# Optimization experiments

Measured on AMD Instinct MI355X. Metric: run time of the kernel, lower is better.

Reference implementation:

```python
import jax, jax.numpy as jnp
import numpy as np

N_HEADS = 8
D_EMBED = 512
D_HEAD = D_EMBED // N_HEADS


def setup_inputs() -> dict:
    key = jax.random.key(0)
    ks = jax.random.split(key, 5)
    x = jax.random.normal(ks[0], (1, 4096, D_EMBED), dtype=jnp.float32)
    # in_proj: Linear(d, 3d); out_proj: Linear(d, d). Stored as [in, out] for x @ W.
    scale_in = 1.0 / np.sqrt(D_EMBED)
    W_in = jax.random.uniform(ks[1], (D_EMBED, 3 * D_EMBED), jnp.float32, -scale_in, scale_in)
    b_in = jax.random.uniform(ks[2], (3 * D_EMBED,), jnp.float32, -scale_in, scale_in)
    W_out = jax.random.uniform(ks[3], (D_EMBED, D_EMBED), jnp.float32, -scale_in, scale_in)
    b_out = jax.random.uniform(ks[4], (D_EMBED,), jnp.float32, -scale_in, scale_in)
    return {"x": x, "W_in": W_in, "b_in": b_in, "W_out": W_out, "b_out": b_out,
            "causal_mask": 1}


def reference(x, W_in, b_in, W_out, b_out, causal_mask):
    B, S, D = x.shape
    qkv = x @ W_in + b_in                      # [B, S, 3D]
    q, k, v = jnp.split(qkv, 3, axis=-1)
    # [B, S, D] -> [B, H, S, d_head]
    def split_heads(t):
        return t.reshape(B, S, N_HEADS, D_HEAD).transpose(0, 2, 1, 3)
    q, k, v = split_heads(q), split_heads(k), split_heads(v)
    weight = jnp.einsum("bhqd,bhkd->bhqk", q, k)  # [B, H, S, S]
    if causal_mask:
        mask = jnp.triu(jnp.ones((S, S), dtype=bool), k=1)
        weight = jnp.where(mask, -jnp.inf, weight)
    weight = weight / jnp.sqrt(jnp.float32(D_HEAD)).astype(weight.dtype)
    weight = jax.nn.softmax(weight, axis=-1)
    out = jnp.einsum("bhqk,bhkd->bhqd", weight, v)  # [B, H, S, d_head]
    out = out.transpose(0, 2, 1, 3).reshape(B, S, D)
    return out @ W_out + b_out
```

## Files before the change

kernel.cpp:

```cpp
#include <hip/hip_runtime.h>
#include <math.h>

#define SEQ 4096
#define DM 512
#define NH 8
#define DH 64
#define TQK (3 * DM)
#define QSCALE 0.18033688011112042f

typedef __attribute__((ext_vector_type(8))) short bf16x8;
typedef __attribute__((ext_vector_type(4))) float floatx4;
typedef unsigned short ushort_t;

__device__ __forceinline__ floatx4 mfma16(bf16x8 a, bf16x8 b, floatx4 c) {
    return __builtin_amdgcn_mfma_f32_16x16x32_bf16(a, b, c, 0, 0, 0);
}
__device__ __forceinline__ float ex2(float x) { return __builtin_amdgcn_exp2f(x); }

__device__ __forceinline__ unsigned int pk2(float a, float b) {
    unsigned int ua = __float_as_uint(a); ua = (ua + 0x7FFFu + ((ua >> 16) & 1u)) >> 16;
    unsigned int ub = __float_as_uint(b); ub = (ub + 0x7FFFu + ((ub >> 16) & 1u)) >> 16;
    return ua | (ub << 16);
}
__device__ __forceinline__ unsigned short f2bf(float x) {
    unsigned int u = __float_as_uint(x);
    return (unsigned short)((u + 0x7FFFu + ((u >> 16) & 1u)) >> 16);
}
__device__ __forceinline__ float bflo(unsigned int u) { return __uint_as_float(u << 16); }
__device__ __forceinline__ float bfhi(unsigned int u) { return __uint_as_float(u & 0xFFFF0000u); }

__device__ __forceinline__ void gload_lds16(const void* g, void* l) {
    __builtin_amdgcn_global_load_lds(
        (const __attribute__((address_space(1))) unsigned int*)g,
        (__attribute__((address_space(3))) unsigned int*)l, 16, 0, 0);
}

#define DPPMAX(x, ctrl) \
    (x) = fmaxf((x), __int_as_float(__builtin_amdgcn_update_dpp(0, __float_as_int(x), (ctrl), 0xF, 0xF, true)))
__device__ __forceinline__ float row_max16(float x) {
    DPPMAX(x, 0xB1);
    DPPMAX(x, 0x4E);
    DPPMAX(x, 0x141);
    DPPMAX(x, 0x140);
    return x;
}

__global__ __launch_bounds__(256) void prep(const float* __restrict__ x,
                                            const float* __restrict__ W_in,
                                            const float* __restrict__ W_out,
                                            ushort_t* __restrict__ xb,
                                            ushort_t* __restrict__ wti,
                                            ushort_t* __restrict__ wto) {
    __shared__ float T[64][65];
    const int bid = blockIdx.x, tid = threadIdx.x;
    if (bid < 1024) {
        const int i = bid * 256 + tid;
        const float4* p = (const float4*)x + (size_t)i * 2;
        float4 f0 = p[0], f1 = p[1];
        ((uint4*)xb)[i] = make_uint4(pk2(f0.x, f0.y), pk2(f0.z, f0.w),
                                     pk2(f1.x, f1.y), pk2(f1.z, f1.w));
        return;
    }
    const float* W; ushort_t* WT; int N, K, n0, k0; bool qscale;
    if (bid < 1216) { int id = bid - 1024; W = W_in;  WT = wti; N = TQK; K = DM;
                      n0 = (id % 24) * 64; k0 = (id / 24) * 64; qscale = true; }
    else            { int id = bid - 1216; W = W_out; WT = wto; N = DM;  K = DM;
                      n0 = (id % 8) * 64;  k0 = (id / 8) * 64;  qscale = false; }
    {
        const int r = tid >> 2, g = tid & 3;
        const float* src = W + (size_t)(k0 + r) * N + n0 + g * 16;
#pragma unroll
        for (int i = 0; i < 4; i++) {
            float4 f = ((const float4*)src)[i];
            T[g * 16 + i * 4 + 0][r] = f.x;
            T[g * 16 + i * 4 + 1][r] = f.y;
            T[g * 16 + i * 4 + 2][r] = f.z;
            T[g * 16 + i * 4 + 3][r] = f.w;
        }
    }
    __syncthreads();
    const int nr = tid >> 2, g2 = tid & 3;
    const float sc = (qscale && (n0 + nr < DM)) ? QSCALE : 1.0f;
    unsigned int pk[8];
#pragma unroll
    for (int j = 0; j < 8; j++)
        pk[j] = pk2(T[nr][g2 * 16 + 2 * j] * sc, T[nr][g2 * 16 + 2 * j + 1] * sc);
    ushort_t* dst = WT + (size_t)(n0 + nr) * K + k0 + g2 * 16;
    ((uint4*)dst)[0] = make_uint4(pk[0], pk[1], pk[2], pk[3]);
    ((uint4*)dst)[1] = make_uint4(pk[4], pk[5], pk[6], pk[7]);
}

__global__ __launch_bounds__(256) void gemm_in(const ushort_t* __restrict__ A,
                                               const ushort_t* __restrict__ BT,
                                               const float* __restrict__ bias,
                                               ushort_t* __restrict__ Cv,
                                               ushort_t* __restrict__ vt_out) {
    __shared__ __align__(16) ushort_t As[2][128 * 64];
    __shared__ __align__(16) ushort_t Bs[2][128 * 64];
    const int tid  = threadIdx.x;
    const int lane = tid & 63;
    const int w    = tid >> 6;
    const int quad = lane >> 4;
    const int ln   = lane & 15;
    const int row0 = blockIdx.y * 128;
    const int col0 = blockIdx.x * 128;
    const int wm = w >> 1, wn = w & 1;
    const int srow = lane >> 3;
    const int js   = (lane & 7) ^ srow;
    const int K = DM, N = TQK;

    floatx4 acc[4][4];
#pragma unroll
    for (int i = 0; i < 4; i++)
#pragma unroll
        for (int j = 0; j < 4; j++) acc[i][j] = (floatx4){0.f, 0.f, 0.f, 0.f};

#pragma unroll
    for (int i = 0; i < 4; i++) {
        const int c = w * 4 + i;
        gload_lds16(A  + (size_t)(row0 + c * 8 + srow) * K + js * 8, &As[0][c * 512]);
        gload_lds16(BT + (size_t)(col0 + c * 8 + srow) * K + js * 8, &Bs[0][c * 512]);
    }

    for (int kt = 0; kt < 8; kt++) {
        const int cur = kt & 1;
        __syncthreads();
        if (kt < 7) {
            const int k0n = (kt + 1) << 6;
#pragma unroll
            for (int i = 0; i < 4; i++) {
                const int c = w * 4 + i;
                gload_lds16(A  + (size_t)(row0 + c * 8 + srow) * K + k0n + js * 8, &As[cur ^ 1][c * 512]);
                gload_lds16(BT + (size_t)(col0 + c * 8 + srow) * K + k0n + js * 8, &Bs[cur ^ 1][c * 512]);
            }
        }
#pragma unroll
        for (int s = 0; s < 2; s++) {
            bf16x8 af[4], bfr[4];
#pragma unroll
            for (int i = 0; i < 4; i++) {
                const int lm = wm * 64 + i * 16 + ln;
                af[i] = *(const bf16x8*)&As[cur][lm * 64 + ((s * 4 + quad) ^ (ln & 7)) * 8];
                const int lnn = wn * 64 + i * 16 + ln;
                bfr[i] = *(const bf16x8*)&Bs[cur][lnn * 64 + ((s * 4 + quad) ^ (ln & 7)) * 8];
            }
#pragma unroll
            for (int i = 0; i < 4; i++)
#pragma unroll
                for (int j = 0; j < 4; j++)
                    acc[i][j] = mfma16(af[i], bfr[j], acc[i][j]);
        }
    }

    if (col0 >= 2 * DM) {
#pragma unroll
        for (int j = 0; j < 4; j++) {
            const int n = col0 + wn * 64 + j * 16 + ln;
            const float bv = bias[n];
#pragma unroll
            for (int i = 0; i < 4; i++) {
                const int mb = row0 + wm * 64 + i * 16 + quad * 4;
                uint2 pkd;
                pkd.x = pk2(acc[i][j][0] + bv, acc[i][j][1] + bv);
                pkd.y = pk2(acc[i][j][2] + bv, acc[i][j][3] + bv);
                *(uint2*)&vt_out[(size_t)(n - 2 * DM) * SEQ + mb] = pkd;
            }
        }
        return;
    }

#pragma unroll
    for (int j = 0; j < 4; j++) {
        const int n = col0 + wn * 64 + j * 16 + ln;
        const float bv = bias[n] * ((n < DM) ? QSCALE : 1.0f);
#pragma unroll
        for (int i = 0; i < 4; i++) {
            const int mb = row0 + wm * 64 + i * 16 + quad * 4;
#pragma unroll
            for (int r = 0; r < 4; r++)
                Cv[(size_t)(mb + r) * N + n] = f2bf(acc[i][j][r] + bv);
        }
    }
}

__global__ __launch_bounds__(512) void attn_split(const ushort_t* __restrict__ qkv_b,
                                                  const ushort_t* __restrict__ vt,
                                                  ushort_t* __restrict__ po,
                                                  float2* __restrict__ pml) {
    __shared__ __align__(16) ushort_t Ks[2][64 * 64];
    __shared__ __align__(16) ushort_t Vs[2][64 * 64];
    __shared__ __align__(16) ushort_t Ps[128 * 72];

    const int tid  = threadIdx.x;
    const int lane = tid & 63;
    const int w    = tid >> 6;
    const int quad = lane >> 4;
    const int ln   = lane & 15;
    const int h    = blockIdx.y;

    const int e = 143 - (int)blockIdx.x;
    int g = 0;
    while (e >= 2 * (g + 1) * (g + 2)) g++;
    const int off = e - 2 * g * (g + 1);
    const int nc  = g + 1;
    const int qt  = 4 * g + off / nc;
    const int c   = off % nc;
    const int T   = 2 * qt + 2;
    const int jt0 = (c * T) / nc;
    const int jt1 = ((c + 1) * T) / nc;
    const int q0  = qt * 128;

    const ushort_t* qrow = qkv_b + (size_t)(q0 + w * 16 + ln) * TQK + h * DH;
    const bf16x8 a0 = *(const bf16x8*)(qrow + quad * 8);
    const bf16x8 a1 = *(const bf16x8*)(qrow + quad * 8 + 32);

    const short oneb = (short)0x3F80;
    const bf16x8 vone = {oneb, oneb, oneb, oneb, oneb, oneb, oneb, oneb};

    float m_q = -INFINITY;
    floatx4 o[4], ol;
#pragma unroll
    for (int t = 0; t < 4; t++) o[t] = (floatx4){0.f, 0.f, 0.f, 0.f};
    ol = (floatx4){0.f, 0.f, 0.f, 0.f};

    const int srow = lane >> 3;
    const int js   = (lane & 7) ^ srow;

    {
        const int k0 = jt0 * 64;
        gload_lds16(qkv_b + (size_t)(k0 + w * 8 + srow) * TQK + DM + h * DH + js * 8,
                    &Ks[0][w * 512]);
        gload_lds16(vt + (size_t)(h * DH + w * 8 + srow) * SEQ + k0 + js * 8,
                    &Vs[0][w * 512]);
    }

    for (int jt = jt0; jt < jt1; ++jt) {
        const int cur = (jt - jt0) & 1;
        const int k0  = jt * 64;
        __syncthreads();
        if (jt + 1 < jt1) {
            const int k0n = (jt + 1) * 64;
            gload_lds16(qkv_b + (size_t)(k0n + w * 8 + srow) * TQK + DM + h * DH + js * 8,
                        &Ks[cur ^ 1][w * 512]);
            gload_lds16(vt + (size_t)(h * DH + w * 8 + srow) * SEQ + k0n + js * 8,
                        &Vs[cur ^ 1][w * 512]);
        }

        floatx4 sa[4];
#pragma unroll
        for (int t = 0; t < 4; t++) {
            const int n = t * 16 + ln;
            const bf16x8 b0 = *(const bf16x8*)&Ks[cur][n * 64 + ((quad) ^ (ln & 7)) * 8];
            const bf16x8 b1 = *(const bf16x8*)&Ks[cur][n * 64 + ((4 + quad) ^ (ln & 7)) * 8];
            floatx4 acc = {0.f, 0.f, 0.f, 0.f};
            acc = mfma16(a0, b0, acc);
            acc = mfma16(a1, b1, acc);
            sa[t] = acc;
        }

        if (k0 + 63 > q0 + w * 16) {
#pragma unroll
            for (int t = 0; t < 4; t++) {
                const int cg2 = k0 + t * 16 + ln;
#pragma unroll
                for (int r = 0; r < 4; r++) {
                    const int rg = q0 + w * 16 + quad * 4 + r;
                    if (cg2 > rg) sa[t][r] = -INFINITY;
                }
            }
        }

        float mx = sa[0][0];
#pragma unroll
        for (int t = 0; t < 4; t++)
#pragma unroll
            for (int r = 0; r < 4; r++) mx = fmaxf(mx, sa[t][r]);
        mx = row_max16(mx);
        const float mn = fmaxf(fmaxf(m_q, mx), -1e30f);
        const float alpha = ex2(m_q - mn);
        m_q = mn;
#pragma unroll
        for (int t = 0; t < 4; t++)
#pragma unroll
            for (int r = 0; r < 4; r++) {
                const float p = ex2(sa[t][r] - mn);
                Ps[(w * 16 + quad * 4 + r) * 72 + t * 16 + ln] =
                    (ushort_t)(__float_as_uint(p) >> 16);
            }
        if (alpha < 1.0f) {
#pragma unroll
            for (int t = 0; t < 4; t++)
#pragma unroll
                for (int r = 0; r < 4; r++) o[t][r] *= alpha;
#pragma unroll
            for (int r = 0; r < 4; r++) ol[r] *= alpha;
        }

        __builtin_amdgcn_wave_barrier();

        const bf16x8 p0 = *(const bf16x8*)&Ps[(w * 16 + ln) * 72 + quad * 8];
        const bf16x8 p1 = *(const bf16x8*)&Ps[(w * 16 + ln) * 72 + quad * 8 + 32];
#pragma unroll
        for (int t = 0; t < 4; t++) {
            const int d = t * 16 + ln;
            const bf16x8 v0 = *(const bf16x8*)&Vs[cur][d * 64 + ((quad) ^ (ln & 7)) * 8];
            const bf16x8 v1 = *(const bf16x8*)&Vs[cur][d * 64 + ((4 + quad) ^ (ln & 7)) * 8];
            o[t] = mfma16(p0, v0, o[t]);
            o[t] = mfma16(p1, v1, o[t]);
        }
        ol = mfma16(p0, vone, ol);
        ol = mfma16(p1, vone, ol);
    }

    const size_t pbase  = ((size_t)h * 144 + e) * (128 * 64);
    const size_t mlbase = ((size_t)h * 144 + e) * 128;
#pragma unroll
    for (int t = 0; t < 4; t++)
#pragma unroll
        for (int r = 0; r < 4; r++)
            po[pbase + (size_t)(w * 16 + quad * 4 + r) * 64 + t * 16 + ln] = f2bf(o[t][r]);
    if (ln == 0) {
#pragma unroll
        for (int r = 0; r < 4; r++)
            pml[mlbase + w * 16 + quad * 4 + r] = make_float2(m_q, ol[r]);
    }
}

__global__ __launch_bounds__(512) void gemm_out(const ushort_t* __restrict__ po,
                                                const float2* __restrict__ pml,
                                                const ushort_t* __restrict__ BT,
                                                const float* __restrict__ bias,
                                                float* __restrict__ out) {
    __shared__ __align__(16) ushort_t As[2][128 * 72];
    __shared__ __align__(16) ushort_t Bs[2][128 * 64];
    const int tid  = threadIdx.x;
    const int lane = tid & 63;
    const int w    = tid >> 6;
    const int quad = lane >> 4;
    const int ln   = lane & 15;
    const int row0 = blockIdx.y * 128;
    const int col0 = blockIdx.x * 128;
    const int wm = w >> 2, wn = w & 3;
    const int srow = lane >> 3;
    const int js   = (lane & 7) ^ srow;

    const int qt = blockIdx.y;
    const int gq = qt >> 2;
    const int nc = gq + 1;
    const int sbase = 2 * gq * (gq + 1) + (qt & 3) * nc;

    const int cr = tid >> 2, cg = tid & 3;

    floatx4 acc[4][2];
#pragma unroll
    for (int i = 0; i < 4; i++)
#pragma unroll
        for (int j = 0; j < 2; j++) acc[i][j] = (floatx4){0.f, 0.f, 0.f, 0.f};

    auto combine = [&](int head, int buf) {
        float2 ml[8];
        float M = -INFINITY;
        for (int ci = 0; ci < nc; ci++) {
            ml[ci] = pml[((size_t)head * 144 + sbase + ci) * 128 + cr];
            M = fmaxf(M, ml[ci].x);
        }
        float L = 0.f;
        float a[16];
#pragma unroll
        for (int j = 0; j < 16; j++) a[j] = 0.f;
        for (int ci = 0; ci < nc; ci++) {
            const float wgt = ex2(ml[ci].x - M);
            L += wgt * ml[ci].y;
            const ushort_t* p = po + ((size_t)head * 144 + sbase + ci) * (128 * 64)
                                   + (size_t)cr * 64 + cg * 16;
            uint4 u0 = ((const uint4*)p)[0];
            uint4 u1 = ((const uint4*)p)[1];
            const unsigned int uu[8] = {u0.x, u0.y, u0.z, u0.w, u1.x, u1.y, u1.z, u1.w};
#pragma unroll
            for (int j = 0; j < 8; j++) {
                a[2 * j]     += wgt * bflo(uu[j]);
                a[2 * j + 1] += wgt * bfhi(uu[j]);
            }
        }
        const float inv = 1.0f / L;
        unsigned int pk[8];
#pragma unroll
        for (int j = 0; j < 8; j++)
            pk[j] = pk2(a[2 * j] * inv, a[2 * j + 1] * inv);
        uint4* dst = (uint4*)&As[buf][cr * 72 + cg * 16];
        dst[0] = make_uint4(pk[0], pk[1], pk[2], pk[3]);
        dst[1] = make_uint4(pk[4], pk[5], pk[6], pk[7]);
    };
    auto loadB = [&](int kt, int buf) {
#pragma unroll
        for (int i = 0; i < 2; i++) {
            const int cgrp = w * 2 + i;
            gload_lds16(BT + (size_t)(col0 + cgrp * 8 + srow) * DM + kt * 64 + js * 8,
                        &Bs[buf][cgrp * 512]);
        }
    };

    loadB(0, 0);
    combine(0, 0);

    for (int kt = 0; kt < 8; kt++) {
        const int cur = kt & 1;
        __syncthreads();
        if (kt < 7) {
            loadB(kt + 1, cur ^ 1);
            combine(kt + 1, cur ^ 1);
        }
#pragma unroll
        for (int s = 0; s < 2; s++) {
            bf16x8 af[4], bfr[2];
#pragma unroll
            for (int i = 0; i < 4; i++) {
                const int lm = wm * 64 + i * 16 + ln;
                af[i] = *(const bf16x8*)&As[cur][lm * 72 + (s * 4 + quad) * 8];
            }
#pragma unroll
            for (int j = 0; j < 2; j++) {
                const int lnn = wn * 32 + j * 16 + ln;
                bfr[j] = *(const bf16x8*)&Bs[cur][lnn * 64 + ((s * 4 + quad) ^ (ln & 7)) * 8];
            }
#pragma unroll
            for (int i = 0; i < 4; i++)
#pragma unroll
                for (int j = 0; j < 2; j++)
                    acc[i][j] = mfma16(af[i], bfr[j], acc[i][j]);
        }
    }

#pragma unroll
    for (int j = 0; j < 2; j++) {
        const int n = col0 + wn * 32 + j * 16 + ln;
        const float bv = bias[n];
#pragma unroll
        for (int i = 0; i < 4; i++) {
            const int mb = row0 + wm * 64 + i * 16 + quad * 4;
#pragma unroll
            for (int r = 0; r < 4; r++)
                out[(size_t)(mb + r) * DM + n] = acc[i][j][r] + bv;
        }
    }
}

extern "C" void kernel_launch(void* const* d_in, const int* in_sizes, int n_in,
                              void* d_out, int out_size, void* d_ws, size_t ws_size,
                              hipStream_t stream) {
    const float* x     = (const float*)d_in[0];
    const float* W_in  = (const float*)d_in[1];
    const float* b_in  = (const float*)d_in[2];
    const float* W_out = (const float*)d_in[3];
    const float* b_out = (const float*)d_in[4];
    float* out = (float*)d_out;

    char* ws = (char*)d_ws;
    ushort_t* xb    = (ushort_t*)ws;
    ushort_t* wti   = (ushort_t*)(ws + (4u  << 20));
    ushort_t* wto   = (ushort_t*)(ws + (6u  << 20));
    ushort_t* qkv_b = (ushort_t*)(ws + (7u  << 20));
    ushort_t* vtb   = (ushort_t*)(ws + (19u << 20));
    ushort_t* po    = (ushort_t*)(ws + (23u << 20));
    float2*   pml   = (float2*)  (ws + (42u << 20));

    prep<<<1280, 256, 0, stream>>>(x, W_in, W_out, xb, wti, wto);

    gemm_in<<<dim3(TQK / 128, SEQ / 128), 256, 0, stream>>>(xb, wti, b_in, qkv_b, vtb);

    attn_split<<<dim3(144, NH), 512, 0, stream>>>(qkv_b, vtb, po, pml);

    gemm_out<<<dim3(DM / 128, SEQ / 128), 512, 0, stream>>>(po, pml, wto, b_out, out);
}
```

Measured before the change: 173.4 us.

## Split split-KV combine out of output GEMM into separate kernel

Moves the flash-decoding style partial-result combine from inside the output projection GEMM into its own attn_combine kernel, which writes a bf16 attention output buffer. The output GEMM becomes a plain pipelined bf16 GEMM with async global-to-LDS loads for both operands, a swizzled A layout, and smaller 128x64 tiles at 256 threads, giving twice as many blocks. This is meant to stop each GEMM block from recomputing the combine serially on its critical path, and to raise parallelism. In exchange it adds a kernel launch and a round trip of the combined activations through global memory.

```diff
diff --git a/kernel.cpp b/kernel.cpp
--- a/kernel.cpp
+++ b/kernel.cpp
@@ -326,89 +326,99 @@
     }
 }
 
-__global__ __launch_bounds__(512) void gemm_out(const ushort_t* __restrict__ po,
-                                                const float2* __restrict__ pml,
+__global__ __launch_bounds__(512) void attn_combine(const ushort_t* __restrict__ po,
+                                                    const float2* __restrict__ pml,
+                                                    ushort_t* __restrict__ aob) {
+    const int qt = blockIdx.x, h = blockIdx.y;
+    const int gq = qt >> 2;
+    const int nc = gq + 1;
+    const int sbase = 2 * gq * (gq + 1) + (qt & 3) * nc;
+    const int row = threadIdx.x >> 2, g = threadIdx.x & 3;
+
+    float2 ml[8];
+    float M = -INFINITY;
+    for (int ci = 0; ci < nc; ci++) {
+        ml[ci] = pml[((size_t)h * 144 + sbase + ci) * 128 + row];
+        M = fmaxf(M, ml[ci].x);
+    }
+    float L = 0.f;
+    float acc[16];
+#pragma unroll
+    for (int j = 0; j < 16; j++) acc[j] = 0.f;
+
+    for (int ci = 0; ci < nc; ci++) {
+        const float wgt = ex2(ml[ci].x - M);
+        L += wgt * ml[ci].y;
+        const ushort_t* p = po + ((size_t)h * 144 + sbase + ci) * (128 * 64)
+                               + (size_t)row * 64 + g * 16;
+        uint4 u0 = ((const uint4*)p)[0];
+        uint4 u1 = ((const uint4*)p)[1];
+        const unsigned int uu[8] = {u0.x, u0.y, u0.z, u0.w, u1.x, u1.y, u1.z, u1.w};
+#pragma unroll
+        for (int j = 0; j < 8; j++) {
+            acc[2 * j]     += wgt * bflo(uu[j]);
+            acc[2 * j + 1] += wgt * bfhi(uu[j]);
+        }
+    }
+    const float inv = 1.0f / L;
+    unsigned int pk[8];
+#pragma unroll
+    for (int j = 0; j < 8; j++)
+        pk[j] = pk2(acc[2 * j] * inv, acc[2 * j + 1] * inv);
+    ushort_t* dst = aob + (size_t)(qt * 128 + row) * DM + h * DH + g * 16;
+    ((uint4*)dst)[0] = make_uint4(pk[0], pk[1], pk[2], pk[3]);
+    ((uint4*)dst)[1] = make_uint4(pk[4], pk[5], pk[6], pk[7]);
+}
+
+__global__ __launch_bounds__(256) void gemm_out(const ushort_t* __restrict__ A,
                                                 const ushort_t* __restrict__ BT,
                                                 const float* __restrict__ bias,
                                                 float* __restrict__ out) {
-    __shared__ __align__(16) ushort_t As[2][128 * 72];
-    __shared__ __align__(16) ushort_t Bs[2][128 * 64];
+    __shared__ __align__(16) ushort_t As[2][128 * 64];
+    __shared__ __align__(16) ushort_t Bs[2][64 * 64];
     const int tid  = threadIdx.x;
     const int lane = tid & 63;
     const int w    = tid >> 6;
     const int quad = lane >> 4;
     const int ln   = lane & 15;
     const int row0 = blockIdx.y * 128;
-    const int col0 = blockIdx.x * 128;
-    const int wm = w >> 2, wn = w & 3;
+    const int col0 = blockIdx.x * 64;
+    const int wm = w >> 1, wn = w & 1;
     const int srow = lane >> 3;
     const int js   = (lane & 7) ^ srow;
 
-    const int qt = blockIdx.y;
-    const int gq = qt >> 2;
-    const int nc = gq + 1;
-    const int sbase = 2 * gq * (gq + 1) + (qt & 3) * nc;
-
-    const int cr = tid >> 2, cg = tid & 3;
-
     floatx4 acc[4][2];
 #pragma unroll
     for (int i = 0; i < 4; i++)
 #pragma unroll
         for (int j = 0; j < 2; j++) acc[i][j] = (floatx4){0.f, 0.f, 0.f, 0.f};
 
-    auto combine = [&](int head, int buf) {
-        float2 ml[8];
-        float M = -INFINITY;
-        for (int ci = 0; ci < nc; ci++) {
-            ml[ci] = pml[((size_t)head * 144 + sbase + ci) * 128 + cr];
-            M = fmaxf(M, ml[ci].x);
-        }
-        float L = 0.f;
-        float a[16];
-#pragma unroll
-        for (int j = 0; j < 16; j++) a[j] = 0.f;
-        for (int ci = 0; ci < nc; ci++) {
-            const float wgt = ex2(ml[ci].x - M);
-            L += wgt * ml[ci].y;
-            const ushort_t* p = po + ((size_t)head * 144 + sbase + ci) * (128 * 64)
-                                   + (size_t)cr * 64 + cg * 16;
-            uint4 u0 = ((const uint4*)p)[0];
-            uint4 u1 = ((const uint4*)p)[1];
-            const unsigned int uu[8] = {u0.x, u0.y, u0.z, u0.w, u1.x, u1.y, u1.z, u1.w};
-#pragma unroll
-            for (int j = 0; j < 8; j++) {
-                a[2 * j]     += wgt * bflo(uu[j]);
-                a[2 * j + 1] += wgt * bfhi(uu[j]);
-            }
-        }
-        const float inv = 1.0f / L;
-        unsigned int pk[8];
-#pragma unroll
-        for (int j = 0; j < 8; j++)
-            pk[j] = pk2(a[2 * j] * inv, a[2 * j + 1] * inv);
-        uint4* dst = (uint4*)&As[buf][cr * 72 + cg * 16];
-        dst[0] = make_uint4(pk[0], pk[1], pk[2], pk[3]);
-        dst[1] = make_uint4(pk[4], pk[5], pk[6], pk[7]);
-    };
-    auto loadB = [&](int kt, int buf) {
-#pragma unroll
-        for (int i = 0; i < 2; i++) {
-            const int cgrp = w * 2 + i;
-            gload_lds16(BT + (size_t)(col0 + cgrp * 8 + srow) * DM + kt * 64 + js * 8,
-                        &Bs[buf][cgrp * 512]);
-        }
-    };
-
-    loadB(0, 0);
-    combine(0, 0);
+#pragma unroll
+    for (int i = 0; i < 4; i++) {
+        const int c = w * 4 + i;
+        gload_lds16(A + (size_t)(row0 + c * 8 + srow) * DM + js * 8, &As[0][c * 512]);
+    }
+#pragma unroll
+    for (int i = 0; i < 2; i++) {
+        const int c = w * 2 + i;
+        gload_lds16(BT + (size_t)(col0 + c * 8 + srow) * DM + js * 8, &Bs[0][c * 512]);
+    }
 
     for (int kt = 0; kt < 8; kt++) {
         const int cur = kt & 1;
         __syncthreads();
         if (kt < 7) {
-            loadB(kt + 1, cur ^ 1);
-            combine(kt + 1, cur ^ 1);
+            const int k0n = (kt + 1) << 6;
+#pragma unroll
+            for (int i = 0; i < 4; i++) {
+                const int c = w * 4 + i;
+                gload_lds16(A + (size_t)(row0 + c * 8 + srow) * DM + k0n + js * 8, &As[cur ^ 1][c * 512]);
+            }
+#pragma unroll
+            for (int i = 0; i < 2; i++) {
+                const int c = w * 2 + i;
+                gload_lds16(BT + (size_t)(col0 + c * 8 + srow) * DM + k0n + js * 8, &Bs[cur ^ 1][c * 512]);
+            }
         }
 #pragma unroll
         for (int s = 0; s < 2; s++) {
@@ -416,7 +426,7 @@
 #pragma unroll
             for (int i = 0; i < 4; i++) {
                 const int lm = wm * 64 + i * 16 + ln;
-                af[i] = *(const bf16x8*)&As[cur][lm * 72 + (s * 4 + quad) * 8];
+                af[i] = *(const bf16x8*)&As[cur][lm * 64 + ((s * 4 + quad) ^ (ln & 7)) * 8];
             }
 #pragma unroll
             for (int j = 0; j < 2; j++) {
@@ -463,6 +473,7 @@
     ushort_t* vtb   = (ushort_t*)(ws + (19u << 20));
     ushort_t* po    = (ushort_t*)(ws + (23u << 20));
     float2*   pml   = (float2*)  (ws + (42u << 20));
+    ushort_t* aob   = (ushort_t*)(ws + (44u << 20));
 
     prep<<<1280, 256, 0, stream>>>(x, W_in, W_out, xb, wti, wto);
 
@@ -470,5 +481,7 @@
 
     attn_split<<<dim3(144, NH), 512, 0, stream>>>(qkv_b, vtb, po, pml);
 
-    gemm_out<<<dim3(DM / 128, SEQ / 128), 512, 0, stream>>>(po, pml, wto, b_out, out);
-}
+    attn_combine<<<dim3(SEQ / 128, NH), 512, 0, stream>>>(po, pml, aob);
+
+    gemm_out<<<dim3(DM / 64, SEQ / 128), 256, 0, stream>>>(aob, wto, b_out, out);
+}
```

Result: faster. 156.0 us, median of 2 (-10.0%).
